# Kernel tuning notes

Hardware: AMD Instinct MI355X
Metric: run time of the kernel (lower is better)

## Reference

```python
import jax, jax.numpy as jnp
import numpy as np

L, B, D, H = 2048, 2, 1024, 16


def setup_inputs() -> dict:
    key = jax.random.key(0)
    ks = jax.random.split(key, 4)
    x = jax.random.normal(ks[0], (L, B, D), dtype=jnp.float32)
    W_in = jax.random.normal(ks[1], (3 * D, D), dtype=jnp.float32) * (1.0 / np.sqrt(D))
    b_in = jnp.zeros((3 * D,), dtype=jnp.float32)
    W_out = jax.random.normal(ks[2], (D, D), dtype=jnp.float32) * (1.0 / np.sqrt(D))
    b_out = jnp.zeros((D,), dtype=jnp.float32)
    mask = jnp.zeros((1, L, L), dtype=jnp.float32)
    return {"q": x, "k": x, "v": x, "mask": mask,
            "W_in": W_in, "b_in": b_in, "W_out": W_out, "b_out": b_out,
            "num_heads": H}


def reference(q, k, v, mask, W_in, b_in, W_out, b_out, num_heads):
    l, b, d = q.shape
    hd = d // num_heads
    # fused QKV projection (q == k == v in this module)
    qkv = q @ W_in.T + b_in                      # (l, b, 3d)
    qh, kh, vh = jnp.split(qkv, 3, axis=-1)      # each (l, b, d)

    def to_heads(t):
        # (l, b, d) -> (b*h, l, hd)
        return t.reshape(l, b * num_heads, hd).transpose(1, 0, 2)

    qh, kh, vh = to_heads(qh), to_heads(kh), to_heads(vh)
    qh = qh / jnp.sqrt(jnp.asarray(hd, dtype=qh.dtype))
    scores = jnp.einsum('nld,nmd->nlm', qh, kh) + mask   # (b*h, l, l)
    attn = jax.nn.softmax(scores, axis=-1)
    z = jnp.einsum('nlm,nmd->nld', attn, vh)             # (b*h, l, hd)
    z = z.transpose(1, 0, 2).reshape(l * b, d)
    z = z @ W_out.T + b_out
    return z.reshape(l, b, d)
```

## Files before the change

kernel.cpp:

```cpp
#include <hip/hip_runtime.h>


typedef short  s8v  __attribute__((ext_vector_type(8)));
typedef short  s4vv __attribute__((ext_vector_type(4)));
typedef float  f4v  __attribute__((ext_vector_type(4)));
typedef float  f4l  __attribute__((ext_vector_type(4)));
typedef float  f16v __attribute__((ext_vector_type(16)));
typedef int    i4v  __attribute__((ext_vector_type(4)));
typedef int    i2v  __attribute__((ext_vector_type(2)));

__device__ __forceinline__ short f2bf(float f) {
  union { float f; unsigned u; } x; x.f = f;
  unsigned r = (x.u + 0x7fffu + ((x.u >> 16) & 1u)) >> 16;
  return (short)r;
}

__device__ __forceinline__ int cvtpk(float lo, float hi) {
  int r;
  asm("v_cvt_pk_bf16_f32 %0, %1, %2" : "=v"(r) : "v"(lo), "v"(hi));
  return r;
}

#define GLDS16(gp, lp) __builtin_amdgcn_global_load_lds( \
    (const __attribute__((address_space(1))) void*)(gp),  \
    (__attribute__((address_space(3))) void*)(lp), 16, 0, 0)

#define LOG2E 1.4426950408889634f

__global__ __launch_bounds__(256) void prep(const float* __restrict__ x,
                                            const float* __restrict__ wi,
                                            const float* __restrict__ wo,
                                            const float* __restrict__ mask,
                                            short* __restrict__ xb,
                                            short* __restrict__ wib,
                                            short* __restrict__ wob,
                                            unsigned* __restrict__ flags) {
  const int b = blockIdx.x;
  if (b < 8192) {
    int i = b * 256 + threadIdx.x;
    const float* src; short* dst; int off;
    if (i < 1048576)               { src = x;  dst = xb;  off = i; }
    else if (i < 1048576 + 786432) { src = wi; dst = wib; off = i - 1048576; }
    else                           { src = wo; dst = wob; off = i - 1835008; }
    f4l v = ((const f4l*)src)[off];
    s4vv o;
    o[0] = f2bf(v[0]); o[1] = f2bf(v[1]); o[2] = f2bf(v[2]); o[3] = f2bf(v[3]);
    ((s4vv*)dst)[off] = o;
  } else {
    const int l = b - 8192;
    const int qt = l >> 7;
    const int t = threadIdx.x;
    const float* row = mask + ((size_t)l << 11) + (t << 3);
    f4l a = *(const f4l*)row;
    f4l bb = *(const f4l*)(row + 4);
    bool nz = (a[0] != 0.f) | (a[1] != 0.f) | (a[2] != 0.f) | (a[3] != 0.f) |
              (bb[0] != 0.f) | (bb[1] != 0.f) | (bb[2] != 0.f) | (bb[3] != 0.f);
    unsigned long long bal = __ballot(nz);
    const int w = t >> 6, lane = t & 63;
    if (lane == 0 && bal) {
      unsigned bits = 0;
#pragma unroll
      for (int g = 0; g < 8; ++g)
        if ((bal >> (g << 3)) & 0xFFull) bits |= 1u << ((w << 3) + g);
      atomicOr(&flags[qt], bits);
    }
  }
}

__global__ __launch_bounds__(512, 1) void gemm_qkv(const short* __restrict__ A,
                                                   const short* __restrict__ B,
                                                   const float* __restrict__ bin,
                                                   short* __restrict__ Qh,
                                                   short* __restrict__ Kh,
                                                   short* __restrict__ VT) {
  __shared__ __align__(16) short As[2][16384];
  __shared__ __align__(16) short Bs[2][16384];
  const int tid = threadIdx.x;
  const int w = tid >> 6, lane = tid & 63;
  const int g = lane >> 4, c15 = lane & 15;
  const int wr = w >> 2, wc = w & 3;
  const int orig = blockIdx.x;
  const int wg = ((orig & 7) * 24) + (orig >> 3);
  const int bx = wg % 12;
  const int by = wg / 12;
  const int rowbase = by << 8;
  const int colbase = bx << 8;
  const int rl = lane >> 3, sp = lane & 7;
  const int swz = (sp ^ rl) << 3;

  f4v acc[8][4] = {};

#define VMW(N) asm volatile("s_waitcnt vmcnt(" #N ")" ::: "memory")
#define BAR()  do { __builtin_amdgcn_s_barrier(); asm volatile("" ::: "memory"); } while (0)

#define STAGE(bi, t) do {                                                        \
    _Pragma("unroll")                                                            \
    for (int c = 0; c < 4; ++c) {                                                \
      const int chunk = (w << 2) + c;                                            \
      const int row = (chunk << 3) + rl;                                         \
      GLDS16(A + ((size_t)(rowbase + row) << 10) + ((t) << 6) + swz,             \
             &As[bi][chunk << 9]);                                               \
      GLDS16(B + ((size_t)(colbase + row) << 10) + ((t) << 6) + swz,             \
             &Bs[bi][chunk << 9]);                                               \
    } } while (0)

  STAGE(0, 0);

#pragma unroll 1
  for (int t = 0; t < 16; ++t) {
    if (t < 15) { STAGE((t + 1) & 1, t + 1); VMW(8); }
    else        { VMW(0); }
    BAR();
    const char* Ac = (const char*)&As[t & 1][0];
    const char* Bc = (const char*)&Bs[t & 1][0];
#pragma unroll
    for (int kk = 0; kk < 2; ++kk) {
      s8v af[8], bf[4];
#pragma unroll
      for (int m = 0; m < 8; ++m) {
        const int row = (wr << 7) + (m << 4) + c15;
        af[m] = *(const s8v*)(Ac + row * 128 + ((((kk << 2) | g) ^ (row & 7)) << 4));
      }
#pragma unroll
      for (int nn = 0; nn < 4; ++nn) {
        const int col = (wc << 6) + (nn << 4) + c15;
        bf[nn] = *(const s8v*)(Bc + col * 128 + ((((kk << 2) | g) ^ (col & 7)) << 4));
      }
#pragma unroll
      for (int m = 0; m < 8; ++m)
#pragma unroll
        for (int nn = 0; nn < 4; ++nn)
          acc[m][nn] = __builtin_amdgcn_mfma_f32_16x16x32_bf16(af[m], bf[nn], acc[m][nn], 0, 0, 0);
    }
    BAR();
  }
#undef STAGE
#undef VMW
#undef BAR

  const int r0 = rowbase + (wr << 7) + (g << 2);
  const int c0 = colbase + (wc << 6) + c15;
  const int which = colbase >> 10;
#pragma unroll
  for (int nn = 0; nn < 4; ++nn) {
    const int col = c0 + (nn << 4);
    const int dd = col & 1023;
    const int hh = dd >> 6, ee = dd & 63;
    const float bias = bin[col];
    if (which == 2) {
      unsigned* v0p = (unsigned*)(VT + ((((size_t)hh << 6) + ee) << 11));
      unsigned* v1p = (unsigned*)(VT + (((((size_t)hh + 16) << 6) + ee) << 11));
#pragma unroll
      for (int m = 0; m < 8; ++m) {
        const int li0 = (r0 >> 1) + (m << 3);
        v0p[li0 >> 1] = (unsigned)cvtpk(acc[m][nn][0] + bias, acc[m][nn][2] + bias);
        v1p[li0 >> 1] = (unsigned)cvtpk(acc[m][nn][1] + bias, acc[m][nn][3] + bias);
      }
    } else {
      const float mul = (which == 0) ? 0.125f * LOG2E : 1.0f;
      short* dst = (which == 0) ? Qh : Kh;
#pragma unroll
      for (int m = 0; m < 8; ++m) {
#pragma unroll
        for (int j = 0; j < 4; ++j) {
          const int row = r0 + (m << 4) + j;
          const int li = row >> 1, bb = row & 1;
          const int nh = (bb << 4) + hh;
          dst[(((size_t)nh * 2048 + li) << 6) + ee] = f2bf((acc[m][nn][j] + bias) * mul);
        }
      }
    }
  }
}

__global__ __launch_bounds__(256) void gemm_out(const short* __restrict__ A,
                                                const short* __restrict__ B,
                                                const float* __restrict__ bout,
                                                float* __restrict__ out) {
  __shared__ __align__(16) short As[128 * 64];
  __shared__ __align__(16) short Bs[64 * 64];
  const int tid = threadIdx.x;
  const int w = tid >> 6, lane = tid & 63;
  const int g = lane >> 4, c15 = lane & 15;
  const int orig = blockIdx.x;
  const int xcd = orig & 7, j6 = orig >> 3;
  const int colblk = (xcd << 1) + (j6 & 1);
  const int rowblk = j6 >> 1;
  const int rowbase = rowblk << 7;
  const int colbase = colblk << 6;
  const int rl = lane >> 3, sp = lane & 7;
  const int swz = (sp ^ rl) << 3;

  f4v acc[2][4] = {};

  for (int kt = 0; kt < 16; ++kt) {
#pragma unroll
    for (int c2 = 0; c2 < 4; ++c2) {
      const int chunk = (w << 2) + c2;
      const int row = (chunk << 3) + rl;
      GLDS16(A + ((size_t)(rowbase + row) << 10) + (kt << 6) + swz, &As[chunk << 9]);
    }
#pragma unroll
    for (int c2 = 0; c2 < 2; ++c2) {
      const int chunk = (w << 1) + c2;
      const int row = (chunk << 3) + rl;
      GLDS16(B + ((size_t)(colbase + row) << 10) + (kt << 6) + swz, &Bs[chunk << 9]);
    }
    __syncthreads();
#pragma unroll
    for (int kk = 0; kk < 2; ++kk) {
      s8v af[2], bf[4];
#pragma unroll
      for (int m = 0; m < 2; ++m) {
        const int row = (w << 5) + (m << 4) + c15;
        af[m] = *(const s8v*)((const char*)As + row * 128 + ((((kk << 2) | g) ^ (row & 7)) << 4));
      }
#pragma unroll
      for (int nn = 0; nn < 4; ++nn) {
        const int col = (nn << 4) + c15;
        bf[nn] = *(const s8v*)((const char*)Bs + col * 128 + ((((kk << 2) | g) ^ (col & 7)) << 4));
      }
#pragma unroll
      for (int m = 0; m < 2; ++m)
#pragma unroll
        for (int nn = 0; nn < 4; ++nn)
          acc[m][nn] = __builtin_amdgcn_mfma_f32_16x16x32_bf16(af[m], bf[nn], acc[m][nn], 0, 0, 0);
    }
    __syncthreads();
  }

  const int r0 = rowbase + (w << 5) + (g << 2);
  const int c0 = colbase + c15;
#pragma unroll
  for (int nn = 0; nn < 4; ++nn) {
    const int col = c0 + (nn << 4);
    const float bias = bout[col];
#pragma unroll
    for (int m = 0; m < 2; ++m) {
#pragma unroll
      for (int j = 0; j < 4; ++j) {
        const int row = r0 + (m << 4) + j;
        out[((size_t)row << 10) + col] = acc[m][nn][j] + bias;
      }
    }
  }
}

__global__ __launch_bounds__(256, 2) void attn(const short* __restrict__ Qh,
                                               const short* __restrict__ Kh,
                                               const short* __restrict__ VTg,
                                               const float* __restrict__ mask,
                                               const unsigned* __restrict__ mflags,
                                               short* __restrict__ Z) {
  __shared__ __align__(16) short Ks[2][128 * 64];
  __shared__ __align__(16) short Vs[2][64 * 128];
  const int tid = threadIdx.x;
  const int w = tid >> 6, lane = tid & 63;
  const int q5 = lane & 31, hi = lane >> 5;
  const int orig = blockIdx.x;
  const int wg = ((orig & 7) << 6) + (orig >> 3);
  const int n = wg >> 4, qt = wg & 15;
  const int krow8 = lane >> 3;
  const int ssw = ((lane & 7) ^ krow8) << 3;
  const int vrow = lane >> 4, vslot = lane & 15;

  const int qg = (qt << 7) + (w << 5) + q5;

  const short* Qp = Qh + (((size_t)n * 2048 + qg) << 6);
  s8v bq[4];
#pragma unroll
  for (int ks = 0; ks < 4; ++ks)
    bq[ks] = *(const s8v*)(Qp + (ks << 4) + (hi << 3));

  const short* Kbase = Kh + ((size_t)n << 17);
  const short* Vbase = VTg + ((size_t)n << 17);
  const float* mrow = mask + ((size_t)qg << 11) + (hi << 2);
  const unsigned mbits = mflags[qt];
  const int kslot = q5 & 7;
  const int vsl15 = q5 & 15;

  f16v oA0, oA1, zz;
#pragma unroll
  for (int e = 0; e < 16; ++e) { oA0[e] = 0.0f; oA1[e] = 0.0f; zz[e] = 0.0f; }
  float ls0 = 0.0f, ls1 = 0.0f;
  f16v sS[4];

#define STAGEK(bi, t) do {                                                      \
    _Pragma("unroll")                                                           \
    for (int c = 0; c < 4; ++c) {                                               \
      const int chunk = (w << 2) + c;                                           \
      GLDS16(Kbase + ((size_t)(((t) << 7) + (chunk << 3) + krow8) << 6) + ssw,  \
             &Ks[bi][chunk << 9]);                                              \
    } } while (0)
#define STAGEV(bi, t) do {                                                      \
    _Pragma("unroll")                                                           \
    for (int c = 0; c < 4; ++c) {                                               \
      const int chunk = (w << 2) + c;                                           \
      const int r = (chunk << 2) + vrow;                                        \
      GLDS16(Vbase + ((size_t)r << 11) + ((t) << 7) + ((vslot ^ (r & 15)) << 3),\
             &Vs[bi][chunk << 9]);                                              \
    } } while (0)

#define QKM(bi) do {                                                            \
    const char* Kc = (const char*)&Ks[bi][0];                                   \
    __builtin_amdgcn_s_setprio(1);                                              \
    _Pragma("unroll")                                                           \
    for (int ks = 0; ks < 4; ++ks) {                                            \
      const int so = ((2 * ks + hi) ^ kslot) << 4;                              \
      s8v a0 = *(const s8v*)(Kc + q5 * 128 + so);                               \
      s8v a1 = *(const s8v*)(Kc + (q5 + 32) * 128 + so);                        \
      s8v a2 = *(const s8v*)(Kc + (q5 + 64) * 128 + so);                        \
      s8v a3 = *(const s8v*)(Kc + (q5 + 96) * 128 + so);                        \
      if (ks == 0) {                                                            \
        sS[0] = __builtin_amdgcn_mfma_f32_32x32x16_bf16(a0, bq[0], zz, 0, 0, 0);\
        sS[1] = __builtin_amdgcn_mfma_f32_32x32x16_bf16(a1, bq[0], zz, 0, 0, 0);\
        sS[2] = __builtin_amdgcn_mfma_f32_32x32x16_bf16(a2, bq[0], zz, 0, 0, 0);\
        sS[3] = __builtin_amdgcn_mfma_f32_32x32x16_bf16(a3, bq[0], zz, 0, 0, 0);\
      } else {                                                                  \
        sS[0] = __builtin_amdgcn_mfma_f32_32x32x16_bf16(a0, bq[ks], sS[0], 0,0,0);\
        sS[1] = __builtin_amdgcn_mfma_f32_32x32x16_bf16(a1, bq[ks], sS[1], 0,0,0);\
        sS[2] = __builtin_amdgcn_mfma_f32_32x32x16_bf16(a2, bq[ks], sS[2], 0,0,0);\
        sS[3] = __builtin_amdgcn_mfma_f32_32x32x16_bf16(a3, bq[ks], sS[3], 0,0,0);\
      } }                                                                       \
    __builtin_amdgcn_s_setprio(0); } while (0)

#define SMPV(t, bi) do {                                                        \
    if ((mbits >> ((t) << 1)) & 1u) {                                           \
      const float* mp = mrow + ((t) << 7);                                      \
      _Pragma("unroll")                                                         \
      for (int c = 0; c < 4; ++c) {                                             \
        f4l m0 = *(const f4l*)(mp + (c << 3));                                  \
        f4l m1 = *(const f4l*)(mp + 32 + (c << 3));                             \
        _Pragma("unroll")                                                       \
        for (int jj = 0; jj < 4; ++jj) {                                        \
          sS[0][(c << 2) + jj] += m0[jj] * LOG2E;                               \
          sS[1][(c << 2) + jj] += m1[jj] * LOG2E;                               \
        } } }                                                                   \
    if ((mbits >> (((t) << 1) + 1)) & 1u) {                                     \
      const float* mp = mrow + ((t) << 7) + 64;                                 \
      _Pragma("unroll")                                                         \
      for (int c = 0; c < 4; ++c) {                                             \
        f4l m0 = *(const f4l*)(mp + (c << 3));                                  \
        f4l m1 = *(const f4l*)(mp + 32 + (c << 3));                             \
        _Pragma("unroll")                                                       \
        for (int jj = 0; jj < 4; ++jj) {                                        \
          sS[2][(c << 2) + jj] += m0[jj] * LOG2E;                               \
          sS[3][(c << 2) + jj] += m1[jj] * LOG2E;                               \
        } } }                                                                   \
    _Pragma("unroll")                                                           \
    for (int r = 0; r < 16; ++r) {                                              \
      float a = __builtin_amdgcn_exp2f(sS[0][r]); sS[0][r] = a; ls0 += a;       \
      float b = __builtin_amdgcn_exp2f(sS[1][r]); sS[1][r] = b; ls1 += b;       \
      float c = __builtin_amdgcn_exp2f(sS[2][r]); sS[2][r] = c; ls0 += c;       \
      float d = __builtin_amdgcn_exp2f(sS[3][r]); sS[3][r] = d; ls1 += d;       \
    }                                                                           \
    const char* Vc = (const char*)&Vs[bi][0];                                   \
    __builtin_amdgcn_s_setprio(1);                                              \
    _Pragma("unroll")                                                           \
    for (int kb = 0; kb < 4; ++kb) {                                            \
      _Pragma("unroll")                                                         \
      for (int ks2 = 0; ks2 < 2; ++ks2) {                                       \
        const int ro = ks2 << 3;                                                \
        int P0 = cvtpk(sS[kb][ro + 0], sS[kb][ro + 1]);                         \
        int P1 = cvtpk(sS[kb][ro + 2], sS[kb][ro + 3]);                         \
        int P2 = cvtpk(sS[kb][ro + 4], sS[kb][ro + 5]);                         \
        int P3 = cvtpk(sS[kb][ro + 6], sS[kb][ro + 7]);                         \
        int x0 = __shfl_xor(P2, 32);                                            \
        int x1 = __shfl_xor(P3, 32);                                            \
        int x2 = __shfl_xor(P0, 32);                                            \
        int x3 = __shfl_xor(P1, 32);                                            \
        union { i4v i; s8v s; } pu;                                             \
        pu.i[0] = hi ? x0 : P0;                                                 \
        pu.i[1] = hi ? x1 : P1;                                                 \
        pu.i[2] = hi ? P2 : x2;                                                 \
        pu.i[3] = hi ? P3 : x3;                                                 \
        const int p = (kb << 1) + ks2;                                          \
        const int so = (((p << 1) + hi) ^ vsl15) << 4;                          \
        s8v av0 = *(const s8v*)(Vc + q5 * 256 + so);                            \
        s8v av1 = *(const s8v*)(Vc + (q5 + 32) * 256 + so);                     \
        oA0 = __builtin_amdgcn_mfma_f32_32x32x16_bf16(av0, pu.s, oA0, 0, 0, 0); \
        oA1 = __builtin_amdgcn_mfma_f32_32x32x16_bf16(av1, pu.s, oA1, 0, 0, 0); \
      } }                                                                       \
    __builtin_amdgcn_s_setprio(0); } while (0)

  STAGEK(0, 0); STAGEV(0, 0);
  __syncthreads();

  for (int t = 0; t < 15; ++t) {
    STAGEK((t + 1) & 1, t + 1);
    STAGEV((t + 1) & 1, t + 1);
    QKM(t & 1);
    SMPV(t, t & 1);
    __syncthreads();
  }
  QKM(1);
  SMPV(15, 1);

#undef STAGEK
#undef STAGEV
#undef QKM
#undef SMPV

  float lrun = ls0 + ls1;
  lrun += __shfl_xor(lrun, 32);
  const float invl = 1.0f / lrun;
  short* zp = Z + ((((size_t)qg << 1) + (n >> 4)) << 10) + ((n & 15) << 6);
#pragma unroll
  for (int c = 0; c < 4; ++c) {
    const int d0 = (c << 3) + (hi << 2);
    i2v w0, w1;
    w0[0] = cvtpk(oA0[(c << 2) + 0] * invl, oA0[(c << 2) + 1] * invl);
    w0[1] = cvtpk(oA0[(c << 2) + 2] * invl, oA0[(c << 2) + 3] * invl);
    *(i2v*)(zp + d0) = w0;
    w1[0] = cvtpk(oA1[(c << 2) + 0] * invl, oA1[(c << 2) + 1] * invl);
    w1[1] = cvtpk(oA1[(c << 2) + 2] * invl, oA1[(c << 2) + 3] * invl);
    *(i2v*)(zp + 32 + d0) = w1;
  }
}

extern "C" void kernel_launch(void* const* d_in, const int* in_sizes, int n_in,
                              void* d_out, int out_size, void* d_ws, size_t ws_size,
                              hipStream_t stream) {
  const float* xq   = (const float*)d_in[0];
  const float* mask = (const float*)d_in[3];
  const float* Win  = (const float*)d_in[4];
  const float* bin  = (const float*)d_in[5];
  const float* Wout = (const float*)d_in[6];
  const float* bout = (const float*)d_in[7];
  float* out = (float*)d_out;

  char* ws = (char*)d_ws;
  short* xb  = (short*)(ws);
  short* wib = (short*)(ws + (8ull  << 20));
  short* wob = (short*)(ws + (14ull << 20));
  short* Qh  = (short*)(ws + (16ull << 20));
  short* Kh  = (short*)(ws + (24ull << 20));
  short* VTg = (short*)(ws + (32ull << 20));
  short* Zb  = (short*)(ws + (40ull << 20));
  unsigned* mflags = (unsigned*)(ws + (48ull << 20));

  hipMemsetAsync(mflags, 0, 16 * sizeof(unsigned), stream);
  prep<<<8192 + 2048, 256, 0, stream>>>(xq, Win, Wout, mask, xb, wib, wob, mflags);
  gemm_qkv<<<192, 512, 0, stream>>>(xb, wib, bin, Qh, Kh, VTg);
  attn<<<512, 256, 0, stream>>>(Qh, Kh, VTg, mask, mflags, Zb);
  gemm_out<<<512, 256, 0, stream>>>(Zb, wob, bout, out);
}
```

Measured before the change: 127.8 us.

## Specialize attention warps into producer load waves and consumer compute waves

The attention kernel grows from 4 to 6 waves per block. Waves 4 and 5 act as dedicated producers that issue all K and V global-to-LDS loads and wait on them, while waves 0-3 only run the QK MFMA, softmax and PV work. This is meant to take load issue and vmcnt waits off the compute waves so copying overlaps compute better. In exchange it raises the register and thread budget per block (launch bounds 384, 2), which may cut occupancy, and it keeps a block-wide barrier every tile.

```diff
diff --git a/kernel.cpp b/kernel.cpp
--- a/kernel.cpp
+++ b/kernel.cpp
@@ -246,7 +246,7 @@
   }
 }
 
-__global__ __launch_bounds__(256, 2) void attn(const short* __restrict__ Qh,
+__global__ __launch_bounds__(384, 2) void attn(const short* __restrict__ Qh,
                                                const short* __restrict__ Kh,
                                                const short* __restrict__ VTg,
                                                const float* __restrict__ mask,
@@ -256,6 +256,7 @@
   __shared__ __align__(16) short Vs[2][64 * 128];
   const int tid = threadIdx.x;
   const int w = tid >> 6, lane = tid & 63;
+  const int wq = w & 3;
   const int q5 = lane & 31, hi = lane >> 5;
   const int orig = blockIdx.x;
   const int wg = ((orig & 7) << 6) + (orig >> 3);
@@ -264,7 +265,7 @@
   const int ssw = ((lane & 7) ^ krow8) << 3;
   const int vrow = lane >> 4, vslot = lane & 15;
 
-  const int qg = (qt << 7) + (w << 5) + q5;
+  const int qg = (qt << 7) + (wq << 5) + q5;
 
   const short* Qp = Qh + (((size_t)n * 2048 + qg) << 6);
   s8v bq[4];
@@ -285,20 +286,20 @@
   float ls0 = 0.0f, ls1 = 0.0f;
   f16v sS[4];
 
-#define STAGEK(bi, t) do {                                                      \
+#define VMW0() asm volatile("s_waitcnt vmcnt(0)" ::: "memory")
+
+#define STAGEK_P(bi, t) do {                                                    \
     _Pragma("unroll")                                                           \
-    for (int c = 0; c < 4; ++c) {                                               \
-      const int chunk = (w << 2) + c;                                           \
-      GLDS16(Kbase + ((size_t)(((t) << 7) + (chunk << 3) + krow8) << 6) + ssw,  \
-             &Ks[bi][chunk << 9]);                                              \
-    } } while (0)
-#define STAGEV(bi, t) do {                                                      \
+    for (int c = 0; c < 16; ++c)                                                \
+      GLDS16(Kbase + ((size_t)(((t) << 7) + (c << 3) + krow8) << 6) + ssw,      \
+             &Ks[bi][c << 9]);                                                  \
+  } while (0)
+#define STAGEV_P(bi, t) do {                                                    \
     _Pragma("unroll")                                                           \
-    for (int c = 0; c < 4; ++c) {                                               \
-      const int chunk = (w << 2) + c;                                           \
-      const int r = (chunk << 2) + vrow;                                        \
+    for (int c = 0; c < 16; ++c) {                                              \
+      const int r = (c << 2) + vrow;                                            \
       GLDS16(Vbase + ((size_t)r << 11) + ((t) << 7) + ((vslot ^ (r & 15)) << 3),\
-             &Vs[bi][chunk << 9]);                                              \
+             &Vs[bi][c << 9]);                                                  \
     } } while (0)
 
 #define QKM(bi) do {                                                            \
@@ -383,38 +384,45 @@
       } }                                                                       \
     __builtin_amdgcn_s_setprio(0); } while (0)
 
-  STAGEK(0, 0); STAGEV(0, 0);
+  if (w == 4)      { STAGEK_P(0, 0); VMW0(); }
+  else if (w == 5) { STAGEV_P(0, 0); VMW0(); }
   __syncthreads();
 
-  for (int t = 0; t < 15; ++t) {
-    STAGEK((t + 1) & 1, t + 1);
-    STAGEV((t + 1) & 1, t + 1);
-    QKM(t & 1);
-    SMPV(t, t & 1);
+#pragma unroll 1
+  for (int t = 0; t < 16; ++t) {
+    if (w == 4) {
+      if (t < 15) { STAGEK_P((t + 1) & 1, t + 1); VMW0(); }
+    } else if (w == 5) {
+      if (t < 15) { STAGEV_P((t + 1) & 1, t + 1); VMW0(); }
+    } else {
+      QKM(t & 1);
+      SMPV(t, t & 1);
+    }
     __syncthreads();
   }
-  QKM(1);
-  SMPV(15, 1);
-
-#undef STAGEK
-#undef STAGEV
+
+#undef STAGEK_P
+#undef STAGEV_P
 #undef QKM
 #undef SMPV
-
-  float lrun = ls0 + ls1;
-  lrun += __shfl_xor(lrun, 32);
-  const float invl = 1.0f / lrun;
-  short* zp = Z + ((((size_t)qg << 1) + (n >> 4)) << 10) + ((n & 15) << 6);
-#pragma unroll
-  for (int c = 0; c < 4; ++c) {
-    const int d0 = (c << 3) + (hi << 2);
-    i2v w0, w1;
-    w0[0] = cvtpk(oA0[(c << 2) + 0] * invl, oA0[(c << 2) + 1] * invl);
-    w0[1] = cvtpk(oA0[(c << 2) + 2] * invl, oA0[(c << 2) + 3] * invl);
-    *(i2v*)(zp + d0) = w0;
-    w1[0] = cvtpk(oA1[(c << 2) + 0] * invl, oA1[(c << 2) + 1] * invl);
-    w1[1] = cvtpk(oA1[(c << 2) + 2] * invl, oA1[(c << 2) + 3] * invl);
-    *(i2v*)(zp + 32 + d0) = w1;
+#undef VMW0
+
+  if (w < 4) {
+    float lrun = ls0 + ls1;
+    lrun += __shfl_xor(lrun, 32);
+    const float invl = 1.0f / lrun;
+    short* zp = Z + ((((size_t)qg << 1) + (n >> 4)) << 10) + ((n & 15) << 6);
+#pragma unroll
+    for (int c = 0; c < 4; ++c) {
+      const int d0 = (c << 3) + (hi << 2);
+      i2v w0, w1;
+      w0[0] = cvtpk(oA0[(c << 2) + 0] * invl, oA0[(c << 2) + 1] * invl);
+      w0[1] = cvtpk(oA0[(c << 2) + 2] * invl, oA0[(c << 2) + 3] * invl);
+      *(i2v*)(zp + d0) = w0;
+      w1[0] = cvtpk(oA1[(c << 2) + 0] * invl, oA1[(c << 2) + 1] * invl);
+      w1[1] = cvtpk(oA1[(c << 2) + 2] * invl, oA1[(c << 2) + 3] * invl);
+      *(i2v*)(zp + 32 + d0) = w1;
+    }
   }
 }
 
@@ -442,6 +450,6 @@
   hipMemsetAsync(mflags, 0, 16 * sizeof(unsigned), stream);
   prep<<<8192 + 2048, 256, 0, stream>>>(xq, Win, Wout, mask, xb, wib, wob, mflags);
   gemm_qkv<<<192, 512, 0, stream>>>(xb, wib, bin, Qh, Kh, VTg);
-  attn<<<512, 256, 0, stream>>>(Qh, Kh, VTg, mask, mflags, Zb);
+  attn<<<512, 384, 0, stream>>>(Qh, Kh, VTg, mask, mflags, Zb);
   gemm_out<<<512, 256, 0, stream>>>(Zb, wob, bout, out);
 }
```

After: 140.0 us. 9.5% more time.
